# Kernel tuning notes

Hardware: AMD Instinct MI355X
Metric: run time of the kernel (lower is better)

## Reference

```python
import jax, jax.numpy as jnp
import numpy as np

D_MODEL = 768
N_HEADS = 12
HEAD_DIM = D_MODEL // N_HEADS
BIAS_HIDDEN = 32


def setup_inputs() -> dict:
    key = jax.random.key(0)
    ks = jax.random.split(key, 16)
    B, L = 4, 1024
    std = 0.02
    inp = {
        "x": jax.random.normal(ks[0], (B, L, D_MODEL), dtype=jnp.float32),
        "spatial_pos": jax.random.uniform(ks[1], (B, L, 2), dtype=jnp.float32),
        "Wq": jax.random.normal(ks[2], (D_MODEL, D_MODEL), dtype=jnp.float32) * std,
        "bq": jnp.zeros((D_MODEL,), dtype=jnp.float32),
        "Wk": jax.random.normal(ks[3], (D_MODEL, D_MODEL), dtype=jnp.float32) * std,
        "bk": jnp.zeros((D_MODEL,), dtype=jnp.float32),
        "Wv": jax.random.normal(ks[4], (D_MODEL, D_MODEL), dtype=jnp.float32) * std,
        "bv": jnp.zeros((D_MODEL,), dtype=jnp.float32),
        "Wo": jax.random.normal(ks[5], (D_MODEL, D_MODEL), dtype=jnp.float32) * std,
        "bo": jnp.zeros((D_MODEL,), dtype=jnp.float32),
        "W1": jax.random.normal(ks[6], (2, BIAS_HIDDEN), dtype=jnp.float32) * 0.5,
        "b1": jnp.zeros((BIAS_HIDDEN,), dtype=jnp.float32),
        "W2": jax.random.normal(ks[7], (BIAS_HIDDEN, N_HEADS), dtype=jnp.float32) * 0.5,
        "b2": jnp.zeros((N_HEADS,), dtype=jnp.float32),
    }
    return inp


def reference(x, spatial_pos, Wq, bq, Wk, bk, Wv, bv, Wo, bo, W1, b1, W2, b2):
    B, L, D = x.shape
    H, hd = N_HEADS, HEAD_DIM
    scale = hd ** (-0.5)

    q = (x @ Wq + bq).reshape(B, L, H, hd)  # [B,L,H,hd]
    k = (x @ Wk + bk).reshape(B, L, H, hd)
    v = (x @ Wv + bv).reshape(B, L, H, hd)

    # scores: [B,H,L,L]
    attn = jnp.einsum("bihd,bjhd->bhij", q, k) * scale

    # pairwise spatial deltas: [B,L,L,2]
    delta = spatial_pos[:, :, None, :] - spatial_pos[:, None, :, :]
    hidden = jax.nn.relu(delta @ W1 + b1)          # [B,L,L,32]
    bias = hidden @ W2 + b2                        # [B,L,L,H]
    attn = attn + jnp.transpose(bias, (0, 3, 1, 2))

    attn = jax.nn.softmax(attn, axis=-1)
    out = jnp.einsum("bhij,bjhd->bihd", attn, v).reshape(B, L, D)
    return out @ Wo + bo
```

## Files before the change

kernel.cpp:

```cpp
#include <hip/hip_runtime.h>
#include <hip/hip_fp16.h>


typedef unsigned short ushort_t;
typedef unsigned int uint_t;
typedef __attribute__((ext_vector_type(8))) short bf16x8;
typedef __attribute__((ext_vector_type(4))) float f32x4;

__device__ __forceinline__ ushort_t f2b(float f) {
    union { float f; uint_t u; } v;
    v.f = f;
    uint_t r = v.u + 0x7fffu + ((v.u >> 16) & 1u);
    return (ushort_t)(r >> 16);
}
__device__ __forceinline__ float b2f(ushort_t b) {
    union { uint_t u; float f; } v;
    v.u = ((uint_t)b) << 16;
    return v.f;
}

__device__ __forceinline__ void gload16(const void* g, void* l) {
    __builtin_amdgcn_global_load_lds(
        (const __attribute__((address_space(1))) unsigned int*)g,
        (__attribute__((address_space(3))) unsigned int*)l, 16, 0, 0);
}

__global__ __launch_bounds__(256) void split_hi_lo(const float* __restrict__ X,
                                                   ushort_t* __restrict__ X2) {
    const int idx = blockIdx.x * 256 + threadIdx.x;
    const int m = idx / 192, k4 = (idx - m * 192) * 4;
    float4 v = *(const float4*)&X[(size_t)m * 768 + k4];
    ushort4 hi, lo;
    hi.x = f2b(v.x); lo.x = f2b(v.x - b2f(hi.x));
    hi.y = f2b(v.y); lo.y = f2b(v.y - b2f(hi.y));
    hi.z = f2b(v.z); lo.z = f2b(v.z - b2f(hi.z));
    hi.w = f2b(v.w); lo.w = f2b(v.w - b2f(hi.w));
    ushort_t* row = X2 + (size_t)m * 2304;
    *(ushort4*)&row[k4]        = hi;
    *(ushort4*)&row[768 + k4]  = hi;
    *(ushort4*)&row[1536 + k4] = lo;
}

__global__ __launch_bounds__(256) void split_wT(const float* __restrict__ W,
                                                ushort_t* __restrict__ Wt,
                                                int n_base) {
    __shared__ float Ws[64][65];
    const int t = threadIdx.x;
    const int rr0 = blockIdx.x * 64, nn0 = blockIdx.y * 64;
    const int c = t & 63, r4 = t >> 6;
#pragma unroll
    for (int e = 0; e < 16; ++e) {
        const int r = r4 + e * 4;
        Ws[r][c] = W[(size_t)(rr0 + r) * 768 + nn0 + c];
    }
    __syncthreads();
#pragma unroll
    for (int e = 0; e < 16; ++e) {
        const int nloc = r4 + e * 4;
        const float v = Ws[c][nloc];
        const ushort_t h = f2b(v);
        const ushort_t l = f2b(v - b2f(h));
        ushort_t* rowp = Wt + (size_t)(n_base + nn0 + nloc) * 2304 + rr0 + c;
        rowp[0]    = h;
        rowp[768]  = l;
        rowp[1536] = h;
    }
}

template <int QKV>
__global__ __launch_bounds__(256) void mfma_gemm(
    const ushort_t* __restrict__ A2, const ushort_t* __restrict__ Bt,
    const float* __restrict__ bv0, const float* __restrict__ bv1,
    const float* __restrict__ bv2, ushort_t* __restrict__ Qh,
    ushort_t* __restrict__ Ql, ushort_t* __restrict__ Kh,
    ushort_t* __restrict__ Kl, ushort_t* __restrict__ Vth,
    ushort_t* __restrict__ Vtl, float* __restrict__ C0) {
    __shared__ ushort_t As[128 * 64];
    __shared__ ushort_t Bs[128 * 64];

    const int t = threadIdx.x;
    const int w = t >> 6, lane = t & 63;
    const int n0 = blockIdx.x * 128, m0 = blockIdx.y * 128;
    const int wr = (w >> 1) * 64, wc = (w & 1) * 64;

    f32x4 acc[4][4];
#pragma unroll
    for (int i = 0; i < 4; ++i)
#pragma unroll
        for (int j = 0; j < 4; ++j) acc[i][j] = (f32x4){0.f, 0.f, 0.f, 0.f};

    const int srow = t >> 3;
    const int sslot = t & 7;

    for (int k0 = 0; k0 < 2304; k0 += 64) {
        __syncthreads();
#pragma unroll
        for (int it = 0; it < 4; ++it) {
            const int row = srow + it * 32;
            const int kk = k0 + (((sslot ^ (row & 7)) << 3));
            char* dstA = (char*)As + it * 4096 + w * 1024;
            char* dstB = (char*)Bs + it * 4096 + w * 1024;
            gload16(A2 + (size_t)(m0 + row) * 2304 + kk, dstA);
            gload16(Bt + (size_t)(n0 + row) * 2304 + kk, dstB);
        }
        __syncthreads();

#pragma unroll
        for (int kk = 0; kk < 2; ++kk) {
            bf16x8 a[4], b[4];
#pragma unroll
            for (int i = 0; i < 4; ++i) {
                const int ra = wr + i * 16 + (lane & 15);
                const int sa = ((kk << 2) + (lane >> 4)) ^ (ra & 7);
                a[i] = *(const bf16x8*)((const char*)As + ra * 128 + sa * 16);
                const int rb = wc + i * 16 + (lane & 15);
                const int sb = ((kk << 2) + (lane >> 4)) ^ (rb & 7);
                b[i] = *(const bf16x8*)((const char*)Bs + rb * 128 + sb * 16);
            }
#pragma unroll
            for (int i = 0; i < 4; ++i)
#pragma unroll
                for (int j = 0; j < 4; ++j)
                    acc[i][j] = __builtin_amdgcn_mfma_f32_16x16x32_bf16(
                        a[i], b[j], acc[i][j], 0, 0, 0);
        }
    }

    const int cl = lane & 15, rg = (lane >> 4) * 4;
    if constexpr (QKV) {
        const int which = n0 / 768;
        const int nb = n0 - which * 768 + wc;
        const float* bb = which == 0 ? bv0 : (which == 1 ? bv1 : bv2);
#pragma unroll
        for (int i = 0; i < 4; ++i)
#pragma unroll
            for (int j = 0; j < 4; ++j) {
                const int cw = nb + j * 16 + cl;
                const int h = cw >> 6, d = cw & 63;
                const float badd = bb[cw];
#pragma unroll
                for (int r = 0; r < 4; ++r) {
                    const int gr = m0 + wr + i * 16 + rg + r;
                    const int b = gr >> 10, l = gr & 1023;
                    const int bh = b * 12 + h;
                    float val = acc[i][j][r] + badd;
                    if (which == 0) val *= 0.125f;
                    const ushort_t hi = f2b(val);
                    const ushort_t lo = f2b(val - b2f(hi));
                    if (which == 0) {
                        const size_t idx = ((size_t)((bh << 10) + l)) * 64 + d;
                        Qh[idx] = hi; Ql[idx] = lo;
                    } else if (which == 1) {
                        const size_t idx = ((size_t)((bh << 10) + l)) * 64 + d;
                        Kh[idx] = hi; Kl[idx] = lo;
                    } else {
                        const size_t idx = (((size_t)((bh << 6) + d)) << 10) + l;
                        Vth[idx] = hi; Vtl[idx] = lo;
                    }
                }
            }
    } else {
#pragma unroll
        for (int i = 0; i < 4; ++i)
#pragma unroll
            for (int j = 0; j < 4; ++j) {
                const int gc = n0 + wc + j * 16 + cl;
#pragma unroll
                for (int r = 0; r < 4; ++r) {
                    const int gr = m0 + wr + i * 16 + rg + r;
                    C0[(size_t)gr * 768 + gc] = acc[i][j][r] + bv0[gc];
                }
            }
    }
}

__global__ __launch_bounds__(256) void bias_mlp(const float* __restrict__ pos,
                                                const float* __restrict__ W1,
                                                const float* __restrict__ b1,
                                                const float* __restrict__ W2,
                                                const float* __restrict__ b2,
                                                __half* __restrict__ Bias) {
    __shared__ float w1x[32], w1y[32], b1s[32], b2s[12];
    __shared__ float w2T[12][32];

    const int t = threadIdx.x;
    const int i = blockIdx.x;
    const int b = blockIdx.y;

    if (t < 32) { w1x[t] = W1[t]; w1y[t] = W1[32 + t]; b1s[t] = b1[t]; }
    if (t >= 32 && t < 44) b2s[t - 32] = b2[t - 32];
    for (int v = t; v < 384; v += 256) {
        const int u = v / 12, hh = v - u * 12;
        w2T[hh][u] = W2[v];
    }
    __syncthreads();

    const float2 pi2 = *(const float2*)&pos[((b << 10) + i) << 1];
    const float4 pj01 = *(const float4*)&pos[((b << 10) + 2 * t) << 1];
    const float4 pj23 = *(const float4*)&pos[((b << 10) + 2 * t + 512) << 1];
    float dx[4], dy[4];
    dx[0] = pi2.x - pj01.x; dy[0] = pi2.y - pj01.y;
    dx[1] = pi2.x - pj01.z; dy[1] = pi2.y - pj01.w;
    dx[2] = pi2.x - pj23.x; dy[2] = pi2.y - pj23.y;
    dx[3] = pi2.x - pj23.z; dy[3] = pi2.y - pj23.w;

    float acc[4][12];
#pragma unroll
    for (int e = 0; e < 4; ++e)
#pragma unroll
        for (int h = 0; h < 12; ++h) acc[e][h] = b2s[h];

#pragma unroll
    for (int u4 = 0; u4 < 8; ++u4) {
        const float4 ax = *(const float4*)&w1x[u4 << 2];
        const float4 ay = *(const float4*)&w1y[u4 << 2];
        const float4 ab = *(const float4*)&b1s[u4 << 2];
        float4 hv[4];
#pragma unroll
        for (int e = 0; e < 4; ++e) {
            hv[e].x = fmaxf(fmaf(dx[e], ax.x, fmaf(dy[e], ay.x, ab.x)), 0.f);
            hv[e].y = fmaxf(fmaf(dx[e], ax.y, fmaf(dy[e], ay.y, ab.y)), 0.f);
            hv[e].z = fmaxf(fmaf(dx[e], ax.z, fmaf(dy[e], ay.z, ab.z)), 0.f);
            hv[e].w = fmaxf(fmaf(dx[e], ax.w, fmaf(dy[e], ay.w, ab.w)), 0.f);
        }
#pragma unroll
        for (int h = 0; h < 12; ++h) {
            const float4 wv = *(const float4*)&w2T[h][u4 << 2];
#pragma unroll
            for (int e = 0; e < 4; ++e)
                acc[e][h] = fmaf(hv[e].x, wv.x,
                            fmaf(hv[e].y, wv.y,
                            fmaf(hv[e].z, wv.z,
                            fmaf(hv[e].w, wv.w, acc[e][h]))));
        }
    }

    const size_t base = (((size_t)(b * 12)) << 20) + (((size_t)i) << 10);
#pragma unroll
    for (int h = 0; h < 12; ++h) {
        const size_t off = base + (((size_t)h) << 20);
        *(__half2*)&Bias[off + 2 * t]       = __floats2half2_rn(acc[0][h], acc[1][h]);
        *(__half2*)&Bias[off + 2 * t + 512] = __floats2half2_rn(acc[2][h], acc[3][h]);
    }
}

__global__ __launch_bounds__(256) void attn_mfma(
    const ushort_t* __restrict__ Qh, const ushort_t* __restrict__ Ql,
    const ushort_t* __restrict__ Kh, const ushort_t* __restrict__ Kl,
    const ushort_t* __restrict__ Vth, const ushort_t* __restrict__ Vtl,
    const __half* __restrict__ BiasT, ushort_t* __restrict__ A2) {
    __shared__ ushort_t Kls[2][64][64];
    __shared__ ushort_t Vls[2][64][64];
    __shared__ ushort_t P2s[4][2][16][64];

    const int t = threadIdx.x;
    const int wgid0 = blockIdx.x;
    const int wgid = (wgid0 & 7) * 96 + (wgid0 >> 3);
    const int bh = wgid >> 4, it = wgid & 15;
    const int b = bh / 12, h = bh - b * 12;
    const int i0 = it << 6;
    const int w = t >> 6, l = t & 63;
    const int l4 = l >> 4, lm = l & 15;

    const __half* bp = BiasT + (((size_t)bh) << 20) +
                       (((size_t)(i0 + 16 * w + l4 * 4)) << 10) + lm;

    const size_t qoff = ((size_t)((bh << 10) + i0 + 16 * w + lm)) * 64 + l4 * 8;
    const bf16x8 qh0 = *(const bf16x8*)(Qh + qoff);
    const bf16x8 qh1 = *(const bf16x8*)(Qh + qoff + 32);
    const bf16x8 ql0 = *(const bf16x8*)(Ql + qoff);
    const bf16x8 ql1 = *(const bf16x8*)(Ql + qoff + 32);

    float m_[4], l_[4];
    f32x4 o_[4];
#pragma unroll
    for (int r = 0; r < 4; ++r) { m_[r] = -1e30f; l_[r] = 0.f; }
#pragma unroll
    for (int db = 0; db < 4; ++db) o_[db] = (f32x4){0.f, 0.f, 0.f, 0.f};

    for (int jt = 0; jt < 16; ++jt) {
        const int j0 = jt << 6;

        float bias_r[4][4];
#pragma unroll
        for (int cb = 0; cb < 4; ++cb)
#pragma unroll
            for (int r = 0; r < 4; ++r)
                bias_r[cb][r] = __half2float(bp[(r << 10) + j0 + 16 * cb]);

        __syncthreads();
        {
            ushort_t* lb = (w == 0) ? &Kls[0][0][0]
                         : (w == 1) ? &Kls[1][0][0]
                         : (w == 2) ? &Vls[0][0][0] : &Vls[1][0][0];
            const ushort_t* gt = (w == 0) ? Kh : (w == 1) ? Kl
                               : (w == 2) ? Vth : Vtl;
#pragma unroll
            for (int ch = 0; ch < 8; ++ch) {
                const int row = ch * 8 + (l >> 3);
                const int off8 = (((l & 7) ^ (row & 7)) << 3);
                const ushort_t* src =
                    (w < 2) ? gt + ((size_t)((bh << 10) + j0 + row)) * 64 + off8
                            : gt + ((size_t)((bh << 6) + row)) * 1024 + j0 + off8;
                gload16(src, (char*)lb + ch * 1024);
            }
        }
        __syncthreads();

        f32x4 s_[4];
#pragma unroll
        for (int cb = 0; cb < 4; ++cb) {
            const int row = 16 * cb + lm;
            const int sw = row & 7;
            const char* k0p = (const char*)&Kls[0][0][0] + row * 128;
            const char* k1p = (const char*)&Kls[1][0][0] + row * 128;
            const bf16x8 kh0 = *(const bf16x8*)(k0p + ((l4 + 0) ^ sw) * 16);
            const bf16x8 kh1 = *(const bf16x8*)(k0p + ((l4 + 4) ^ sw) * 16);
            const bf16x8 kl0 = *(const bf16x8*)(k1p + ((l4 + 0) ^ sw) * 16);
            const bf16x8 kl1 = *(const bf16x8*)(k1p + ((l4 + 4) ^ sw) * 16);
            f32x4 a = (f32x4){0.f, 0.f, 0.f, 0.f};
            a = __builtin_amdgcn_mfma_f32_16x16x32_bf16(qh0, kh0, a, 0, 0, 0);
            a = __builtin_amdgcn_mfma_f32_16x16x32_bf16(qh1, kh1, a, 0, 0, 0);
            a = __builtin_amdgcn_mfma_f32_16x16x32_bf16(qh0, kl0, a, 0, 0, 0);
            a = __builtin_amdgcn_mfma_f32_16x16x32_bf16(qh1, kl1, a, 0, 0, 0);
            a = __builtin_amdgcn_mfma_f32_16x16x32_bf16(ql0, kh0, a, 0, 0, 0);
            a = __builtin_amdgcn_mfma_f32_16x16x32_bf16(ql1, kh1, a, 0, 0, 0);
            s_[cb] = a;
        }

#pragma unroll
        for (int cb = 0; cb < 4; ++cb)
#pragma unroll
            for (int r = 0; r < 4; ++r) s_[cb][r] += bias_r[cb][r];

        float corr[4];
#pragma unroll
        for (int r = 0; r < 4; ++r) {
            float mx = fmaxf(fmaxf(s_[0][r], s_[1][r]), fmaxf(s_[2][r], s_[3][r]));
            mx = fmaxf(mx, __shfl_xor(mx, 1));
            mx = fmaxf(mx, __shfl_xor(mx, 2));
            mx = fmaxf(mx, __shfl_xor(mx, 4));
            mx = fmaxf(mx, __shfl_xor(mx, 8));
            const float mn = fmaxf(m_[r], mx);
            corr[r] = __expf(m_[r] - mn);
            m_[r] = mn;
            float ps = 0.f;
#pragma unroll
            for (int cb = 0; cb < 4; ++cb) {
                s_[cb][r] = __expf(s_[cb][r] - mn);
                ps += s_[cb][r];
            }
            ps += __shfl_xor(ps, 1);
            ps += __shfl_xor(ps, 2);
            ps += __shfl_xor(ps, 4);
            ps += __shfl_xor(ps, 8);
            l_[r] = fmaf(l_[r], corr[r], ps);
            o_[0][r] *= corr[r]; o_[1][r] *= corr[r];
            o_[2][r] *= corr[r]; o_[3][r] *= corr[r];
        }

        char* pw = (char*)&P2s[w][0][0][0];
#pragma unroll
        for (int cb = 0; cb < 4; ++cb)
#pragma unroll
            for (int r = 0; r < 4; ++r) {
                const float p = s_[cb][r];
                const ushort_t ph = f2b(p);
                const ushort_t pl = f2b(p - b2f(ph));
                const int rl = l4 * 4 + r;
                const int bo = rl * 128 + ((((lm >> 3) + 2 * cb) ^ (rl & 7)) << 4)
                               + ((2 * lm) & 15);
                *(ushort_t*)(pw + bo) = ph;
                *(ushort_t*)(pw + 2048 + bo) = pl;
            }

        const int psw = lm & 7;
        const char* pb = (const char*)&P2s[w][0][0][0] + lm * 128;
        const bf16x8 pa0 = *(const bf16x8*)(pb + ((l4 + 0) ^ psw) * 16);
        const bf16x8 pa1 = *(const bf16x8*)(pb + ((l4 + 4) ^ psw) * 16);
        const bf16x8 pb0 = *(const bf16x8*)(pb + 2048 + ((l4 + 0) ^ psw) * 16);
        const bf16x8 pb1 = *(const bf16x8*)(pb + 2048 + ((l4 + 4) ^ psw) * 16);

#pragma unroll
        for (int db = 0; db < 4; ++db) {
            const int vrow = 16 * db + lm;
            const int vw = vrow & 7;
            const char* v0p = (const char*)&Vls[0][0][0] + vrow * 128;
            const char* v1p = (const char*)&Vls[1][0][0] + vrow * 128;
            const bf16x8 vh0 = *(const bf16x8*)(v0p + ((l4 + 0) ^ vw) * 16);
            const bf16x8 vh1 = *(const bf16x8*)(v0p + ((l4 + 4) ^ vw) * 16);
            const bf16x8 vl0 = *(const bf16x8*)(v1p + ((l4 + 0) ^ vw) * 16);
            const bf16x8 vl1 = *(const bf16x8*)(v1p + ((l4 + 4) ^ vw) * 16);
            f32x4 a = o_[db];
            a = __builtin_amdgcn_mfma_f32_16x16x32_bf16(pa0, vh0, a, 0, 0, 0);
            a = __builtin_amdgcn_mfma_f32_16x16x32_bf16(pa1, vh1, a, 0, 0, 0);
            a = __builtin_amdgcn_mfma_f32_16x16x32_bf16(pa0, vl0, a, 0, 0, 0);
            a = __builtin_amdgcn_mfma_f32_16x16x32_bf16(pa1, vl1, a, 0, 0, 0);
            a = __builtin_amdgcn_mfma_f32_16x16x32_bf16(pb0, vh0, a, 0, 0, 0);
            a = __builtin_amdgcn_mfma_f32_16x16x32_bf16(pb1, vh1, a, 0, 0, 0);
            o_[db] = a;
        }
    }

    const int mrow = (b << 10) + i0 + 16 * w + l4 * 4;
#pragma unroll
    for (int r = 0; r < 4; ++r) {
        const float inv = 1.f / l_[r];
        ushort_t* rowp = A2 + (size_t)(mrow + r) * 2304;
#pragma unroll
        for (int db = 0; db < 4; ++db) {
            const float val = o_[db][r] * inv;
            const ushort_t hi = f2b(val);
            const ushort_t lo = f2b(val - b2f(hi));
            const int c = (h << 6) + 16 * db + lm;
            rowp[c] = hi;
            rowp[768 + c] = hi;
            rowp[1536 + c] = lo;
        }
    }
}

extern "C" void kernel_launch(void* const* d_in, const int* in_sizes, int n_in,
                              void* d_out, int out_size, void* d_ws, size_t ws_size,
                              hipStream_t stream) {
    const float* x   = (const float*)d_in[0];
    const float* pos = (const float*)d_in[1];
    const float* Wq  = (const float*)d_in[2];
    const float* bq  = (const float*)d_in[3];
    const float* Wk  = (const float*)d_in[4];
    const float* bk  = (const float*)d_in[5];
    const float* Wv  = (const float*)d_in[6];
    const float* bv  = (const float*)d_in[7];
    const float* Wo  = (const float*)d_in[8];
    const float* bo  = (const float*)d_in[9];
    const float* W1  = (const float*)d_in[10];
    const float* b1  = (const float*)d_in[11];
    const float* W2  = (const float*)d_in[12];
    const float* b2  = (const float*)d_in[13];
    float* out = (float*)d_out;

    ushort_t* Qhb = (ushort_t*)d_ws;
    ushort_t* Qlb = Qhb + 3145728;
    ushort_t* Khb = Qlb + 3145728;
    ushort_t* Klb = Khb + 3145728;
    ushort_t* Vth = Klb + 3145728;
    ushort_t* Vtl = Vth + 3145728;
    ushort_t* A2  = Vtl + 3145728;
    ushort_t* W2b = A2 + 9437184;
    __half* BiasH = (__half*)(W2b + 5308416);

    split_hi_lo<<<3072, 256, 0, stream>>>(x, A2);
    split_wT<<<dim3(12, 12), 256, 0, stream>>>(Wq, W2b, 0);
    split_wT<<<dim3(12, 12), 256, 0, stream>>>(Wk, W2b, 768);
    split_wT<<<dim3(12, 12), 256, 0, stream>>>(Wv, W2b, 1536);

    mfma_gemm<1><<<dim3(18, 32), 256, 0, stream>>>(
        A2, W2b, bq, bk, bv, Qhb, Qlb, Khb, Klb, Vth, Vtl, nullptr);

    bias_mlp<<<dim3(1024, 4), 256, 0, stream>>>(pos, W1, b1, W2, b2, BiasH);

    attn_mfma<<<768, 256, 0, stream>>>(Qhb, Qlb, Khb, Klb, Vth, Vtl, BiasH, A2);

    split_wT<<<dim3(12, 12), 256, 0, stream>>>(Wo, W2b, 0);
    mfma_gemm<0><<<dim3(6, 32), 256, 0, stream>>>(
        A2, W2b, bo, nullptr, nullptr, nullptr, nullptr, nullptr, nullptr, nullptr,
        nullptr, out);
}
```

Measured before the change: 374.3 us.

## Store hi/lo once and remap K-phases; double-buffer GEMM LDS with tile swizzle

Split-bf16 operands are now stored as [hi|lo] (1536 columns) instead of the duplicated [hi|hi|lo] layout (2304 columns). A kmap function builds the three hi*hi, hi*lo and lo*hi K-phases by offsetting into the A and B halves. This cuts operand memory traffic and the writes in the split kernels and the attention epilogue. The GEMM also gains double-buffered LDS with a prefetch of the next stage before compute, plus a block-index remap for better L2 locality, at the cost of twice the LDS footprint.

```diff
diff --git a/kernel.cpp b/kernel.cpp
--- a/kernel.cpp
+++ b/kernel.cpp
@@ -35,10 +35,9 @@
     hi.y = f2b(v.y); lo.y = f2b(v.y - b2f(hi.y));
     hi.z = f2b(v.z); lo.z = f2b(v.z - b2f(hi.z));
     hi.w = f2b(v.w); lo.w = f2b(v.w - b2f(hi.w));
-    ushort_t* row = X2 + (size_t)m * 2304;
-    *(ushort4*)&row[k4]        = hi;
-    *(ushort4*)&row[768 + k4]  = hi;
-    *(ushort4*)&row[1536 + k4] = lo;
+    ushort_t* row = X2 + (size_t)m * 1536;
+    *(ushort4*)&row[k4]       = hi;
+    *(ushort4*)&row[768 + k4] = lo;
 }
 
 __global__ __launch_bounds__(256) void split_wT(const float* __restrict__ W,
@@ -60,11 +59,17 @@
         const float v = Ws[c][nloc];
         const ushort_t h = f2b(v);
         const ushort_t l = f2b(v - b2f(h));
-        ushort_t* rowp = Wt + (size_t)(n_base + nn0 + nloc) * 2304 + rr0 + c;
-        rowp[0]    = h;
-        rowp[768]  = l;
-        rowp[1536] = h;
-    }
+        ushort_t* rowp = Wt + (size_t)(n_base + nn0 + nloc) * 1536 + rr0 + c;
+        rowp[0]   = h;
+        rowp[768] = l;
+    }
+}
+
+__device__ __forceinline__ void kmap(int s, int& ka, int& kb) {
+    const int phase = s / 12;
+    const int q = s - phase * 12;
+    ka = ((phase == 2) ? 768 : 0) + q * 64;
+    kb = ((phase == 1) ? 768 : 0) + q * 64;
 }
 
 template <int QKV>
@@ -75,12 +80,19 @@
     ushort_t* __restrict__ Ql, ushort_t* __restrict__ Kh,
     ushort_t* __restrict__ Kl, ushort_t* __restrict__ Vth,
     ushort_t* __restrict__ Vtl, float* __restrict__ C0) {
-    __shared__ ushort_t As[128 * 64];
-    __shared__ ushort_t Bs[128 * 64];
+    __shared__ ushort_t As[2][128 * 64];
+    __shared__ ushort_t Bs[2][128 * 64];
 
     const int t = threadIdx.x;
     const int w = t >> 6, lane = t & 63;
-    const int n0 = blockIdx.x * 128, m0 = blockIdx.y * 128;
+
+    const int nbx = QKV ? 18 : 6;
+    const int lid0 = blockIdx.y * nbx + blockIdx.x;
+    const int cpx = (nbx * 32) >> 3;
+    const int lid = (lid0 & 7) * cpx + (lid0 >> 3);
+    const int n0 = (lid % nbx) * 128;
+    const int m0 = (lid / nbx) * 128;
+
     const int wr = (w >> 1) * 64, wc = (w & 1) * 64;
 
     f32x4 acc[4][4];
@@ -92,19 +104,19 @@
     const int srow = t >> 3;
     const int sslot = t & 7;
 
-    for (int k0 = 0; k0 < 2304; k0 += 64) {
-        __syncthreads();
+    auto STAGE = [&](int buf, int ka, int kb) {
 #pragma unroll
         for (int it = 0; it < 4; ++it) {
             const int row = srow + it * 32;
-            const int kk = k0 + (((sslot ^ (row & 7)) << 3));
-            char* dstA = (char*)As + it * 4096 + w * 1024;
-            char* dstB = (char*)Bs + it * 4096 + w * 1024;
-            gload16(A2 + (size_t)(m0 + row) * 2304 + kk, dstA);
-            gload16(Bt + (size_t)(n0 + row) * 2304 + kk, dstB);
-        }
-        __syncthreads();
-
+            const int sw8 = ((sslot ^ (row & 7)) << 3);
+            char* dstA = (char*)&As[buf][0] + it * 4096 + w * 1024;
+            char* dstB = (char*)&Bs[buf][0] + it * 4096 + w * 1024;
+            gload16(A2 + (size_t)(m0 + row) * 1536 + ka + sw8, dstA);
+            gload16(Bt + (size_t)(n0 + row) * 1536 + kb + sw8, dstB);
+        }
+    };
+
+    auto COMPUTE = [&](int buf) {
 #pragma unroll
         for (int kk = 0; kk < 2; ++kk) {
             bf16x8 a[4], b[4];
@@ -112,10 +124,10 @@
             for (int i = 0; i < 4; ++i) {
                 const int ra = wr + i * 16 + (lane & 15);
                 const int sa = ((kk << 2) + (lane >> 4)) ^ (ra & 7);
-                a[i] = *(const bf16x8*)((const char*)As + ra * 128 + sa * 16);
+                a[i] = *(const bf16x8*)((const char*)&As[buf][0] + ra * 128 + sa * 16);
                 const int rb = wc + i * 16 + (lane & 15);
                 const int sb = ((kk << 2) + (lane >> 4)) ^ (rb & 7);
-                b[i] = *(const bf16x8*)((const char*)Bs + rb * 128 + sb * 16);
+                b[i] = *(const bf16x8*)((const char*)&Bs[buf][0] + rb * 128 + sb * 16);
             }
 #pragma unroll
             for (int i = 0; i < 4; ++i)
@@ -124,7 +136,21 @@
                     acc[i][j] = __builtin_amdgcn_mfma_f32_16x16x32_bf16(
                         a[i], b[j], acc[i][j], 0, 0, 0);
         }
-    }
+    };
+
+    int ka, kb;
+    kmap(0, ka, kb);
+    STAGE(0, ka, kb);
+    __syncthreads();
+    int cur = 0;
+    for (int s = 0; s < 35; ++s) {
+        kmap(s + 1, ka, kb);
+        STAGE(cur ^ 1, ka, kb);
+        COMPUTE(cur);
+        __syncthreads();
+        cur ^= 1;
+    }
+    COMPUTE(cur);
 
     const int cl = lane & 15, rg = (lane >> 4) * 4;
     if constexpr (QKV) {
@@ -406,7 +432,7 @@
 #pragma unroll
     for (int r = 0; r < 4; ++r) {
         const float inv = 1.f / l_[r];
-        ushort_t* rowp = A2 + (size_t)(mrow + r) * 2304;
+        ushort_t* rowp = A2 + (size_t)(mrow + r) * 1536;
 #pragma unroll
         for (int db = 0; db < 4; ++db) {
             const float val = o_[db][r] * inv;
@@ -414,8 +440,7 @@
             const ushort_t lo = f2b(val - b2f(hi));
             const int c = (h << 6) + 16 * db + lm;
             rowp[c] = hi;
-            rowp[768 + c] = hi;
-            rowp[1536 + c] = lo;
+            rowp[768 + c] = lo;
         }
     }
 }
@@ -446,8 +471,8 @@
     ushort_t* Vth = Klb + 3145728;
     ushort_t* Vtl = Vth + 3145728;
     ushort_t* A2  = Vtl + 3145728;
-    ushort_t* W2b = A2 + 9437184;
-    __half* BiasH = (__half*)(W2b + 5308416);
+    ushort_t* W2b = A2 + 6291456;
+    __half* BiasH = (__half*)(W2b + 3538944);
 
     split_hi_lo<<<3072, 256, 0, stream>>>(x, A2);
     split_wT<<<dim3(12, 12), 256, 0, stream>>>(Wq, W2b, 0);
```

Result: slower. 393.8 us (+5.2%).
